# Optimization experiments

Hardware: AMD Instinct MI355X
Metric: run time of the kernel (lower is better)

The kernel has to match this reference:

```python
import jax, jax.numpy as jnp
import numpy as np

EPS = 1e-6
INPUTS = 1836
LABELS = 159
NUM_VALS = 2
HIDDEN = 1024
BATCH = 8192
ITERS = 20          # cfg.inference.iterations
INF_LR = 1.0        # cfg.inference.learning_rate (sqrt decay)
ENT_COEF = 1.0      # cfg.entropy_coef


def setup_inputs() -> dict:
    key = jax.random.key(0)
    ks = jax.random.split(key, 8)
    f32 = jnp.float32
    xs = jax.random.normal(ks[0], (BATCH, INPUTS), f32)
    # feature MLP: 1836 -> 150 -> 150 -> 159 (weights ~ N(0, 2/fan_in), bias 0)
    Wf1 = jax.random.normal(ks[1], (150, INPUTS), f32) * np.sqrt(2.0 / INPUTS).astype(np.float32)
    bf1 = jnp.zeros((150,), f32)
    Wf2 = jax.random.normal(ks[2], (150, 150), f32) * np.sqrt(2.0 / 150).astype(np.float32)
    bf2 = jnp.zeros((150,), f32)
    Wf3 = jax.random.normal(ks[3], (LABELS, 150), f32) * np.sqrt(2.0 / 150).astype(np.float32)
    bf3 = jnp.zeros((LABELS,), f32)
    # global energy net: Linear(159->1024, no bias), Softplus, Linear(1024->1, no bias)
    Wg1 = jax.random.normal(ks[4], (HIDDEN, LABELS), f32) * (1.0 / np.sqrt(LABELS)).astype(np.float32)
    Wg2 = jax.random.normal(ks[5], (1, HIDDEN), f32) * (1.0 / np.sqrt(HIDDEN)).astype(np.float32)
    return dict(xs=xs, Wf1=Wf1, bf1=bf1, Wf2=Wf2, bf2=bf2, Wf3=Wf3, bf3=bf3, Wg1=Wg1, Wg2=Wg2)


def _init_pred(batch_size):
    # _random_probabilities: sorted-uniform stick-breaking, shared across the batch
    x = jax.random.uniform(jax.random.key(1), (LABELS, NUM_VALS + 1), jnp.float32)
    x = x.at[:, 0].set(0.0).at[:, -1].set(1.0)
    x = jnp.sort(x, axis=1)
    p = x[:, 1:] - x[:, :-1]                       # (LABELS, NUM_VALS), rows sum to 1
    return jnp.broadcast_to(p[None], (batch_size, LABELS, NUM_VALS))


def reference(xs, Wf1, bf1, Wf2, bf2, Wf3, bf3, Wg1, Wg2):
    # feature energy network -> potentials (B, LABELS, 2), channel 0 is zero
    h = jax.nn.relu(xs @ Wf1.T + bf1)
    h = jax.nn.relu(h @ Wf2.T + bf2)
    logits = h @ Wf3.T + bf3                        # (B, LABELS)
    potentials = jnp.stack([jnp.zeros_like(logits), logits], axis=-1)  # (B, LABELS, 2)

    def energy_sum(pred):
        # sum over batch of: <pred, potentials> + Wg2 softplus(Wg1 pred[:,:,1]) - c*H-term
        ge = jnp.sum(pred * potentials)
        le = jnp.sum(jax.nn.softplus(pred[:, :, 1] @ Wg1.T) @ Wg2.T)
        ent = jnp.sum(pred * jnp.log(pred + EPS))
        return ge + le - ENT_COEF * ent

    egrad = jax.grad(energy_sum)

    def step(pred, it):
        g = egrad(pred)                             # (B, LABELS, NUM_VALS)
        lr = INF_LR / jnp.sqrt(it.astype(jnp.float32))
        lg = lr * g
        m = jnp.max(lg, axis=-1, keepdims=True)     # stabilized multiplicative update
        p = pred * jnp.exp(lg - m)
        p = p / (jnp.sum(p, axis=-1, keepdims=True) + EPS)
        return p, None

    pred0 = _init_pred(xs.shape[0])
    pred, _ = jax.lax.scan(step, pred0, jnp.arange(1, ITERS))
    return pred
```

## Files before the change

### kernel.cpp

```cpp
#include <hip/hip_runtime.h>
#include <hip/hip_bf16.h>
#include <math.h>

#define EPSF 1e-6f
#define NLBL 159
#define NLP  160
#define HID  1024
#define BATCH 8192
#define MROWS 32
#define PBS  168
#define SBS  1044
#define K1   1836
#define K1P  1856
#define NF   150
#define NFP  160

typedef __attribute__((ext_vector_type(8))) short short8v;
typedef __attribute__((ext_vector_type(4))) float f32x4;

__device__ inline ushort f2bf(float f) {
  __hip_bfloat16 h = __float2bfloat16(f);
  return *reinterpret_cast<ushort*>(&h);
}
__device__ inline float bf2f(ushort u) {
  unsigned v = ((unsigned)u) << 16;
  return __uint_as_float(v);
}
__device__ inline float rcpf(float x) { return __builtin_amdgcn_rcpf(x); }
__device__ inline float sigmoidf(float x) { return rcpf(1.0f + __expf(-x)); }

__device__ inline unsigned rotl32(unsigned x, int d){ return (x<<d)|(x>>(32-d)); }

__device__ inline void threefry2x32(unsigned k0, unsigned k1,
                                    unsigned x0, unsigned x1,
                                    unsigned* o0, unsigned* o1) {
  unsigned ks0=k0, ks1=k1, ks2=k0^k1^0x1BD11BDAu;
  x0 += ks0; x1 += ks1;
#define TF_R(r) { x0 += x1; x1 = rotl32(x1,(r)); x1 ^= x0; }
  TF_R(13) TF_R(15) TF_R(26) TF_R(6)  x0 += ks1; x1 += ks2 + 1u;
  TF_R(17) TF_R(29) TF_R(16) TF_R(24) x0 += ks2; x1 += ks0 + 2u;
  TF_R(13) TF_R(15) TF_R(26) TF_R(6)  x0 += ks0; x1 += ks1 + 3u;
  TF_R(17) TF_R(29) TF_R(16) TF_R(24) x0 += ks1; x1 += ks2 + 4u;
  TF_R(13) TF_R(15) TF_R(26) TF_R(6)  x0 += ks2; x1 += ks0 + 5u;
#undef TF_R
  *o0 = x0; *o1 = x1;
}

template<int RELU>
__global__ __launch_bounds__(256) void gemm_xwt(const float* __restrict__ A,
                                                const float* __restrict__ W,
                                                const float* __restrict__ bias,
                                                float* __restrict__ C,
                                                int M, int N, int K) {
  __shared__ float As[32][68];
  __shared__ float Ws[32][68];
  const int tid = threadIdx.x;
  const int m0 = blockIdx.x * 64;
  const int n0 = blockIdx.y * 64;
  const int tn = tid & 15;
  const int tm = tid >> 4;
  float acc[4][4];
#pragma unroll
  for (int i=0;i<4;++i)
#pragma unroll
    for (int j=0;j<4;++j) acc[i][j]=0.f;

  for (int k0 = 0; k0 < K; k0 += 32) {
    __syncthreads();
#pragma unroll
    for (int s2 = 0; s2 < 8; ++s2) {
      int f = tid + s2*256;
      int kk = f & 31, mm = f >> 5;
      int k = k0 + kk;
      float av = 0.f, wvv = 0.f;
      if (k < K) {
        av = A[(size_t)(m0+mm)*K + k];
        int n = n0 + mm;
        if (n < N) wvv = W[(size_t)n*K + k];
      }
      As[kk][mm] = av;
      Ws[kk][mm] = wvv;
    }
    __syncthreads();
    for (int kk=0; kk<32; ++kk) {
      float4 a4 = *(const float4*)&As[kk][tm*4];
      float4 b4 = *(const float4*)&Ws[kk][tn*4];
      float ai[4] = {a4.x,a4.y,a4.z,a4.w};
      float bj[4] = {b4.x,b4.y,b4.z,b4.w};
#pragma unroll
      for (int i=0;i<4;++i)
#pragma unroll
        for (int j=0;j<4;++j) acc[i][j] = fmaf(ai[i], bj[j], acc[i][j]);
    }
  }
#pragma unroll
  for (int i=0;i<4;++i)
#pragma unroll
    for (int j=0;j<4;++j) {
      int m = m0 + tm*4 + i;
      int n = n0 + tn*4 + j;
      if (n < N) {
        float v = acc[i][j] + bias[n];
        if (RELU) v = fmaxf(v, 0.f);
        C[(size_t)m*N + n] = v;
      }
    }
}

__global__ void prep_weights(const float* __restrict__ Wg1,
                             ushort* __restrict__ Wg1b,
                             ushort* __restrict__ Wg1Tb) {
  int idx = blockIdx.x*256 + threadIdx.x;
  if (idx >= HID*NLP) return;
  int h = idx / NLP, l = idx % NLP;
  float v = (l < NLBL) ? Wg1[h*NLBL + l] : 0.f;
  ushort b = f2bf(v);
  Wg1b[h*NLP + l]  = b;
  Wg1Tb[l*HID + h] = b;
}

__global__ void prep_wf1(const float* __restrict__ Wf1,
                         ushort* __restrict__ Wh, ushort* __restrict__ Wl) {
  int idx = blockIdx.x*256 + threadIdx.x;
  if (idx >= NFP*K1P) return;
  int n = idx / K1P, k = idx % K1P;
  float v = (n < NF && k < K1) ? Wf1[n*K1 + k] : 0.f;
  ushort h = f2bf(v);
  Wh[idx] = h;
  Wl[idx] = f2bf(v - bf2f(h));
}

__global__ __launch_bounds__(256) void gemm1_split(
    const float* __restrict__ xs, const ushort* __restrict__ Wh,
    const ushort* __restrict__ Wl, const float* __restrict__ bias,
    float* __restrict__ h1) {
  __shared__ float Asf[32*36];
  const int tid = threadIdx.x;
  const int wv = tid >> 6, lane = tid & 63;
  const int c = lane & 15, g = lane >> 4;
  const int row0 = blockIdx.x * 32;
  const int ntc = (wv < 2) ? 3 : 2;
  const int ntv[3] = {wv, wv + 4, wv + 8};

  f32x4 acc[3][2];
#pragma unroll
  for (int t = 0; t < 3; ++t)
#pragma unroll
    for (int rt = 0; rt < 2; ++rt) acc[t][rt] = (f32x4){0.f,0.f,0.f,0.f};

  const int srow = tid >> 3;
  const int skof = (tid & 7) * 4;

  for (int ks = 0; ks < K1P/32; ++ks) {
    const int k0 = ks * 32;
    const int ksrc = k0 + skof;
    const float4 av = *(const float4*)&xs[(size_t)(row0 + srow)*K1 + ((ksrc < K1) ? ksrc : 0)];
    __syncthreads();
    *(float4*)&Asf[srow*36 + skof] = av;
    __syncthreads();
    short8v ah[2], al[2];
#pragma unroll
    for (int rt = 0; rt < 2; ++rt) {
      const float* ap = &Asf[(rt*16 + c)*36 + g*8];
      float4 x0 = *(const float4*)ap;
      float4 x1 = *(const float4*)(ap + 4);
      float xv[8] = {x0.x,x0.y,x0.z,x0.w,x1.x,x1.y,x1.z,x1.w};
#pragma unroll
      for (int j = 0; j < 8; ++j) {
        ushort hh = f2bf(xv[j]);
        ah[rt][j] = (short)hh;
        al[rt][j] = (short)f2bf(xv[j] - bf2f(hh));
      }
    }
#pragma unroll
    for (int t = 0; t < 3; ++t) {
      if (t >= ntc) break;
      const int n = ntv[t]*16 + c;
      const size_t wo = (size_t)n*K1P + k0 + g*8;
      short8v wh = *(const short8v*)&Wh[wo];
      short8v wl = *(const short8v*)&Wl[wo];
#pragma unroll
      for (int rt = 0; rt < 2; ++rt) {
        acc[t][rt] = __builtin_amdgcn_mfma_f32_16x16x32_bf16(ah[rt], wh, acc[t][rt], 0, 0, 0);
        acc[t][rt] = __builtin_amdgcn_mfma_f32_16x16x32_bf16(ah[rt], wl, acc[t][rt], 0, 0, 0);
        acc[t][rt] = __builtin_amdgcn_mfma_f32_16x16x32_bf16(al[rt], wh, acc[t][rt], 0, 0, 0);
      }
    }
  }
#pragma unroll
  for (int t = 0; t < 3; ++t) {
    if (t >= ntc) break;
    const int n = ntv[t]*16 + c;
    if (n < NF) {
      const float bv = bias[n];
#pragma unroll
      for (int rt = 0; rt < 2; ++rt)
#pragma unroll
        for (int r = 0; r < 4; ++r) {
          int m = row0 + rt*16 + g*4 + r;
          h1[(size_t)m*NF + n] = fmaxf(acc[t][rt][r] + bv, 0.f);
        }
    }
  }
}

__global__ __launch_bounds__(512, 2) void spen_iter_mfma(
    const float* __restrict__ logits,
    const ushort* __restrict__ Wg1b,
    const ushort* __restrict__ Wg1Tb,
    const float* __restrict__ Wg2,
    float* __restrict__ out) {
  __shared__ ushort p1b[MROWS*PBS];
  __shared__ ushort s_b[MROWS*SBS];
  __shared__ float  u_s[NLBL];

  const int tid  = threadIdx.x;
  const int wv   = tid >> 6;
  const int lane = tid & 63;
  const int col  = lane & 15;
  const int kg   = lane >> 4;
  const int row0 = blockIdx.x * MROWS;

  if (tid < NLBL) {
    unsigned i = 3u*(unsigned)tid + 1u;
    unsigned x0, x1; bool use1;
    if (i < 239u) { x0 = i; x1 = (i == 238u) ? 0u : (239u + i); use1 = false; }
    else          { x0 = i - 239u; x1 = i; use1 = true; }
    unsigned o0, o1;
    threefry2x32(0u, 1u, x0, x1, &o0, &o1);
    unsigned bits = use1 ? o1 : o0;
    u_s[tid] = __uint_as_float((bits >> 9) | 0x3f800000u) - 1.0f;
  }
  __syncthreads();
  for (int idx = tid; idx < MROWS*NLP; idx += 512) {
    int m = idx / NLP, l = idx % NLP;
    float p1 = (l < NLBL) ? (1.0f - u_s[l]) : 0.f;
    p1b[m*PBS + l] = f2bf(p1);
  }

  const bool has2 = (wv < 2);
  const int l0 = wv*16 + col;
  const int l1 = 128 + wv*16 + col;
  const bool v1 = has2 && (l1 < NLBL);

  float q0[8], q1[8];
  {
    float u0v = u_s[l0];
    float qi0 = __logf((1.0f - u0v) * rcpf(u0v));
    float qi1 = 0.f;
    if (v1) { float u1v = u_s[l1]; qi1 = __logf((1.0f - u1v) * rcpf(u1v)); }
#pragma unroll
    for (int i = 0; i < 8; ++i) { q0[i] = qi0; q1[i] = qi1; }
  }

  float wg2own[8];
#pragma unroll
  for (int tt = 0; tt < 8; ++tt) wg2own[tt] = Wg2[(wv*8 + tt)*16 + col];

  float lg0[8], lg1[8];
#pragma unroll
  for (int rh = 0; rh < 2; ++rh)
#pragma unroll
    for (int r = 0; r < 4; ++r) {
      int m = row0 + rh*16 + kg*4 + r;
      lg0[rh*4+r] = logits[(size_t)m*NLBL + l0];
      lg1[rh*4+r] = v1 ? logits[(size_t)m*NLBL + l1] : 0.f;
    }

  const ushort* wbase = Wg1b + ((size_t)(wv*8)*16 + col)*NLP + kg*8;

  for (int it = 1; it <= 19; ++it) {
    const float lr = rsqrtf((float)it);
    __syncthreads();
    short8v afr0[5], afr1[5];
#pragma unroll
    for (int kk = 0; kk < 5; ++kk) {
      afr0[kk] = *(const short8v*)&p1b[col*PBS + kk*32 + kg*8];
      afr1[kk] = *(const short8v*)&p1b[(16 + col)*PBS + kk*32 + kg*8];
    }
    short8v wA[2][5];
#pragma unroll
    for (int kk = 0; kk < 5; ++kk) wA[0][kk] = *(const short8v*)(wbase + kk*32);
#pragma unroll
    for (int tt = 0; tt < 8; ++tt) {
      const int cur = tt & 1;
      if (tt < 7) {
        const ushort* wp = wbase + (size_t)((tt + 1)*16)*NLP;
#pragma unroll
        for (int kk = 0; kk < 5; ++kk) wA[cur^1][kk] = *(const short8v*)(wp + kk*32);
      }
      f32x4 a0 = (f32x4){0.f,0.f,0.f,0.f};
      f32x4 a1 = (f32x4){0.f,0.f,0.f,0.f};
#pragma unroll
      for (int kk = 0; kk < 5; ++kk) {
        a0 = __builtin_amdgcn_mfma_f32_16x16x32_bf16(afr0[kk], wA[cur][kk], a0, 0, 0, 0);
        a1 = __builtin_amdgcn_mfma_f32_16x16x32_bf16(afr1[kk], wA[cur][kk], a1, 0, 0, 0);
      }
      const int h = (wv*8 + tt)*16 + col;
      const float wg2v = wg2own[tt];
#pragma unroll
      for (int r = 0; r < 4; ++r) {
        s_b[(kg*4 + r)*SBS + h]      = f2bf(wg2v * sigmoidf(a0[r]));
        s_b[(16 + kg*4 + r)*SBS + h] = f2bf(wg2v * sigmoidf(a1[r]));
      }
    }
    __syncthreads();
    f32x4 bA0 = (f32x4){0.f,0.f,0.f,0.f};
    f32x4 bA1 = (f32x4){0.f,0.f,0.f,0.f};
    f32x4 bB0 = (f32x4){0.f,0.f,0.f,0.f};
    f32x4 bB1 = (f32x4){0.f,0.f,0.f,0.f};
    const ushort* sp0 = &s_b[col*SBS + kg*8];
    const ushort* sp1 = &s_b[(16 + col)*SBS + kg*8];
    const ushort* wt0 = &Wg1Tb[(size_t)l0*HID + kg*8];
    if (has2) {
      const ushort* wt1 = &Wg1Tb[(size_t)l1*HID + kg*8];
#pragma unroll
      for (int kk = 0; kk < 32; ++kk) {
        short8v w0 = *(const short8v*)(wt0 + kk*32);
        short8v w1 = *(const short8v*)(wt1 + kk*32);
        short8v a0 = *(const short8v*)(sp0 + kk*32);
        short8v a1 = *(const short8v*)(sp1 + kk*32);
        bA0 = __builtin_amdgcn_mfma_f32_16x16x32_bf16(a0, w0, bA0, 0, 0, 0);
        bA1 = __builtin_amdgcn_mfma_f32_16x16x32_bf16(a1, w0, bA1, 0, 0, 0);
        bB0 = __builtin_amdgcn_mfma_f32_16x16x32_bf16(a0, w1, bB0, 0, 0, 0);
        bB1 = __builtin_amdgcn_mfma_f32_16x16x32_bf16(a1, w1, bB1, 0, 0, 0);
      }
    } else {
#pragma unroll
      for (int kk = 0; kk < 32; ++kk) {
        short8v w0 = *(const short8v*)(wt0 + kk*32);
        short8v a0 = *(const short8v*)(sp0 + kk*32);
        short8v a1 = *(const short8v*)(sp1 + kk*32);
        bA0 = __builtin_amdgcn_mfma_f32_16x16x32_bf16(a0, w0, bA0, 0, 0, 0);
        bA1 = __builtin_amdgcn_mfma_f32_16x16x32_bf16(a1, w0, bA1, 0, 0, 0);
      }
    }
#define UPDATE_ONE(QARR, IDX, LGV, BK, LL, MM)                               \
    {                                                                        \
      float q = QARR[IDX];                                                   \
      float p1v = sigmoidf(q);                                               \
      float p0v = 1.0f - p1v;                                                \
      float rp1 = rcpf(p1v + EPSF);                                          \
      float rp0 = rcpf(p0v + EPSF);                                          \
      float dlt = (LGV) + (BK) - __logf((p1v + EPSF)*rp0) - p1v*rp1 + p0v*rp0;\
      q += lr*dlt;                                                           \
      QARR[IDX] = q;                                                         \
      p1b[(MM)*PBS + (LL)] = f2bf(sigmoidf(q));                              \
    }
#pragma unroll
    for (int r = 0; r < 4; ++r) {
      const int m0r = kg*4 + r;
      UPDATE_ONE(q0, r, lg0[r], bA0[r], l0, m0r)
      const int m1r = 16 + kg*4 + r;
      UPDATE_ONE(q0, 4 + r, lg0[4 + r], bA1[r], l0, m1r)
    }
    if (v1) {
#pragma unroll
      for (int r = 0; r < 4; ++r) {
        const int m0r = kg*4 + r;
        UPDATE_ONE(q1, r, lg1[r], bB0[r], l1, m0r)
        const int m1r = 16 + kg*4 + r;
        UPDATE_ONE(q1, 4 + r, lg1[4 + r], bB1[r], l1, m1r)
      }
    }
#undef UPDATE_ONE
  }

#pragma unroll
  for (int rh = 0; rh < 2; ++rh)
#pragma unroll
    for (int r = 0; r < 4; ++r) {
      const int row = row0 + rh*16 + kg*4 + r;
      float p1v = sigmoidf(q0[rh*4 + r]);
      size_t o = ((size_t)row*NLBL + l0)*2;
      out[o]   = 1.0f - p1v;
      out[o+1] = p1v;
      if (v1) {
        float p1w = sigmoidf(q1[rh*4 + r]);
        size_t o2 = ((size_t)row*NLBL + l1)*2;
        out[o2]   = 1.0f - p1w;
        out[o2+1] = p1w;
      }
    }
}

extern "C" void kernel_launch(void* const* d_in, const int* in_sizes, int n_in,
                              void* d_out, int out_size, void* d_ws, size_t ws_size,
                              hipStream_t stream) {
  const float* xs  = (const float*)d_in[0];
  const float* Wf1 = (const float*)d_in[1];
  const float* bf1 = (const float*)d_in[2];
  const float* Wf2 = (const float*)d_in[3];
  const float* bf2 = (const float*)d_in[4];
  const float* Wf3 = (const float*)d_in[5];
  const float* bf3 = (const float*)d_in[6];
  const float* Wg1 = (const float*)d_in[7];
  const float* Wg2 = (const float*)d_in[8];
  float* out = (float*)d_out;

  float* h1     = (float*)d_ws;
  float* h2     = h1 + (size_t)BATCH*NF;
  float* logits = h2 + (size_t)BATCH*NF;
  ushort* Wg1b  = (ushort*)(logits + (size_t)BATCH*NLBL);
  ushort* Wg1Tb = Wg1b + (size_t)HID*NLP;
  ushort* Wf1h  = Wg1Tb + (size_t)NLP*HID;
  ushort* Wf1l  = Wf1h + (size_t)NFP*K1P;

  prep_wf1<<<(NFP*K1P + 255)/256, 256, 0, stream>>>(Wf1, Wf1h, Wf1l);
  prep_weights<<<(HID*NLP + 255)/256, 256, 0, stream>>>(Wg1, Wg1b, Wg1Tb);

  gemm1_split<<<BATCH/32, 256, 0, stream>>>(xs, Wf1h, Wf1l, bf1, h1);
  gemm_xwt<1><<<dim3(BATCH/64, 3), 256, 0, stream>>>(h1, Wf2, bf2, h2, BATCH, NF, NF);
  gemm_xwt<0><<<dim3(BATCH/64, 3), 256, 0, stream>>>(h2, Wf3, bf3, logits, BATCH, NLBL, NF);

  spen_iter_mfma<<<BATCH/MROWS, 512, 0, stream>>>(logits, Wg1b, Wg1Tb, Wg2, out);
}
```

Before: 525.5 us.

## Rebalance hidden-tile split across waves and skew weight-load order per block

Phase A's 64 hidden tiles are now split unevenly between waves. The two waves that also carry a second label tile in phase B get only 2 tiles, and the other six get 10 each. This balances the combined MFMA work per wave. Weight loads in both phases are skewed by block index, so blocks running at the same time read different parts of Wg1 and stagger cache and channel pressure. Phase B now prefetches weights in double-buffered chunks of four, which adds register pressure under the existing launch bounds.

Result: slower. 596.5 us (+13.5%).

```diff
diff --git a/kernel.cpp b/kernel.cpp
--- a/kernel.cpp
+++ b/kernel.cpp
@@ -204,6 +204,103 @@
   }
 }
 
+template<int NPAIR>
+__device__ __forceinline__ void phase_a(
+    const ushort* __restrict__ wbase,
+    const float* __restrict__ Wg2,
+    const short8v afr0[5], const short8v afr1[5],
+    ushort* __restrict__ s_b,
+    int col, int kg, int tstart, int pskew)
+{
+  short8v wb[2][2][5];
+  float   wgp[2][2];
+  {
+    const int pv = pskew;
+    const ushort* b0 = wbase + (size_t)((tstart + pv*2)*16)*NLP;
+#pragma unroll
+    for (int kk = 0; kk < 5; ++kk) {
+      wb[0][0][kk] = *(const short8v*)(b0 + kk*32);
+      wb[0][1][kk] = *(const short8v*)(b0 + (size_t)16*NLP + kk*32);
+    }
+    wgp[0][0] = Wg2[(tstart + pv*2)*16 + col];
+    wgp[0][1] = Wg2[(tstart + pv*2 + 1)*16 + col];
+  }
+#pragma unroll
+  for (int p = 0; p < NPAIR; ++p) {
+    const int cur = p & 1;
+    int pv = p + pskew; if (pv >= NPAIR) pv -= NPAIR;
+    if (p + 1 < NPAIR) {
+      int pn = p + 1 + pskew; if (pn >= NPAIR) pn -= NPAIR;
+      const ushort* b1 = wbase + (size_t)((tstart + pn*2)*16)*NLP;
+#pragma unroll
+      for (int kk = 0; kk < 5; ++kk) {
+        wb[cur^1][0][kk] = *(const short8v*)(b1 + kk*32);
+        wb[cur^1][1][kk] = *(const short8v*)(b1 + (size_t)16*NLP + kk*32);
+      }
+      wgp[cur^1][0] = Wg2[(tstart + pn*2)*16 + col];
+      wgp[cur^1][1] = Wg2[(tstart + pn*2 + 1)*16 + col];
+    }
+#pragma unroll
+    for (int i = 0; i < 2; ++i) {
+      f32x4 a0 = (f32x4){0.f,0.f,0.f,0.f};
+      f32x4 a1 = (f32x4){0.f,0.f,0.f,0.f};
+#pragma unroll
+      for (int kk = 0; kk < 5; ++kk) {
+        a0 = __builtin_amdgcn_mfma_f32_16x16x32_bf16(afr0[kk], wb[cur][i][kk], a0, 0, 0, 0);
+        a1 = __builtin_amdgcn_mfma_f32_16x16x32_bf16(afr1[kk], wb[cur][i][kk], a1, 0, 0, 0);
+      }
+      const int h = (tstart + pv*2 + i)*16 + col;
+      const float g = wgp[cur][i];
+#pragma unroll
+      for (int r = 0; r < 4; ++r) {
+        s_b[(kg*4 + r)*SBS + h]      = f2bf(g * sigmoidf(a0[r]));
+        s_b[(16 + kg*4 + r)*SBS + h] = f2bf(g * sigmoidf(a1[r]));
+      }
+    }
+  }
+}
+
+template<int NLT>
+__device__ __forceinline__ void phase_b(
+    const ushort* __restrict__ wt0, const ushort* __restrict__ wt1,
+    const ushort* __restrict__ sp0, const ushort* __restrict__ sp1,
+    int bskew, f32x4 (&acc)[2][2])
+{
+  short8v wr[2][NLT][4];
+  {
+    const int kc = bskew * 4;
+#pragma unroll
+    for (int j = 0; j < 4; ++j) {
+      wr[0][0][j] = *(const short8v*)(wt0 + (kc + j)*32);
+      if (NLT == 2) wr[0][NLT-1][j] = *(const short8v*)(wt1 + (kc + j)*32);
+    }
+  }
+#pragma unroll
+  for (int kb = 0; kb < 8; ++kb) {
+    const int cur = kb & 1;
+    if (kb + 1 < 8) {
+      const int kn = ((kb + 1 + bskew) & 7) * 4;
+#pragma unroll
+      for (int j = 0; j < 4; ++j) {
+        wr[cur^1][0][j] = *(const short8v*)(wt0 + (kn + j)*32);
+        if (NLT == 2) wr[cur^1][NLT-1][j] = *(const short8v*)(wt1 + (kn + j)*32);
+      }
+    }
+    const int kc = ((kb + bskew) & 7) * 4;
+#pragma unroll
+    for (int j = 0; j < 4; ++j) {
+      short8v a0 = *(const short8v*)(sp0 + (kc + j)*32);
+      short8v a1 = *(const short8v*)(sp1 + (kc + j)*32);
+      acc[0][0] = __builtin_amdgcn_mfma_f32_16x16x32_bf16(a0, wr[cur][0][j], acc[0][0], 0, 0, 0);
+      acc[0][1] = __builtin_amdgcn_mfma_f32_16x16x32_bf16(a1, wr[cur][0][j], acc[0][1], 0, 0, 0);
+      if (NLT == 2) {
+        acc[1][0] = __builtin_amdgcn_mfma_f32_16x16x32_bf16(a0, wr[cur][NLT-1][j], acc[1][0], 0, 0, 0);
+        acc[1][1] = __builtin_amdgcn_mfma_f32_16x16x32_bf16(a1, wr[cur][NLT-1][j], acc[1][1], 0, 0, 0);
+      }
+    }
+  }
+}
+
 __global__ __launch_bounds__(512, 2) void spen_iter_mfma(
     const float* __restrict__ logits,
     const ushort* __restrict__ Wg1b,
@@ -220,6 +317,8 @@
   const int col  = lane & 15;
   const int kg   = lane >> 4;
   const int row0 = blockIdx.x * MROWS;
+  const int pskew5 = (int)((blockIdx.x >> 3) % 5u);
+  const int bskew  = (int)((blockIdx.x >> 3) & 7u);
 
   if (tid < NLBL) {
     unsigned i = 3u*(unsigned)tid + 1u;
@@ -242,6 +341,7 @@
   const int l0 = wv*16 + col;
   const int l1 = 128 + wv*16 + col;
   const bool v1 = has2 && (l1 < NLBL);
+  const int tstart = (wv < 2) ? wv*2 : 4 + (wv - 2)*10;
 
   float q0[8], q1[8];
   {
@@ -253,10 +353,6 @@
     for (int i = 0; i < 8; ++i) { q0[i] = qi0; q1[i] = qi1; }
   }
 
-  float wg2own[8];
-#pragma unroll
-  for (int tt = 0; tt < 8; ++tt) wg2own[tt] = Wg2[(wv*8 + tt)*16 + col];
-
   float lg0[8], lg1[8];
 #pragma unroll
   for (int rh = 0; rh < 2; ++rh)
@@ -267,7 +363,11 @@
       lg1[rh*4+r] = v1 ? logits[(size_t)m*NLBL + l1] : 0.f;
     }
 
-  const ushort* wbase = Wg1b + ((size_t)(wv*8)*16 + col)*NLP + kg*8;
+  const ushort* wbase = Wg1b + (size_t)col*NLP + kg*8;
+  const ushort* sp0 = &s_b[col*SBS + kg*8];
+  const ushort* sp1 = &s_b[(16 + col)*SBS + kg*8];
+  const ushort* wt0 = &Wg1Tb[(size_t)l0*HID + kg*8];
+  const ushort* wt1 = &Wg1Tb[(size_t)l1*HID + kg*8];
 
   for (int it = 1; it <= 19; ++it) {
     const float lr = rsqrtf((float)it);
@@ -278,63 +378,16 @@
       afr0[kk] = *(const short8v*)&p1b[col*PBS + kk*32 + kg*8];
       afr1[kk] = *(const short8v*)&p1b[(16 + col)*PBS + kk*32 + kg*8];
     }
-    short8v wA[2][5];
-#pragma unroll
-    for (int kk = 0; kk < 5; ++kk) wA[0][kk] = *(const short8v*)(wbase + kk*32);
-#pragma unroll
-    for (int tt = 0; tt < 8; ++tt) {
-      const int cur = tt & 1;
-      if (tt < 7) {
-        const ushort* wp = wbase + (size_t)((tt + 1)*16)*NLP;
-#pragma unroll
-        for (int kk = 0; kk < 5; ++kk) wA[cur^1][kk] = *(const short8v*)(wp + kk*32);
-      }
-      f32x4 a0 = (f32x4){0.f,0.f,0.f,0.f};
-      f32x4 a1 = (f32x4){0.f,0.f,0.f,0.f};
-#pragma unroll
-      for (int kk = 0; kk < 5; ++kk) {
-        a0 = __builtin_amdgcn_mfma_f32_16x16x32_bf16(afr0[kk], wA[cur][kk], a0, 0, 0, 0);
-        a1 = __builtin_amdgcn_mfma_f32_16x16x32_bf16(afr1[kk], wA[cur][kk], a1, 0, 0, 0);
-      }
-      const int h = (wv*8 + tt)*16 + col;
-      const float wg2v = wg2own[tt];
-#pragma unroll
-      for (int r = 0; r < 4; ++r) {
-        s_b[(kg*4 + r)*SBS + h]      = f2bf(wg2v * sigmoidf(a0[r]));
-        s_b[(16 + kg*4 + r)*SBS + h] = f2bf(wg2v * sigmoidf(a1[r]));
-      }
-    }
-    __syncthreads();
-    f32x4 bA0 = (f32x4){0.f,0.f,0.f,0.f};
-    f32x4 bA1 = (f32x4){0.f,0.f,0.f,0.f};
-    f32x4 bB0 = (f32x4){0.f,0.f,0.f,0.f};
-    f32x4 bB1 = (f32x4){0.f,0.f,0.f,0.f};
-    const ushort* sp0 = &s_b[col*SBS + kg*8];
-    const ushort* sp1 = &s_b[(16 + col)*SBS + kg*8];
-    const ushort* wt0 = &Wg1Tb[(size_t)l0*HID + kg*8];
-    if (has2) {
-      const ushort* wt1 = &Wg1Tb[(size_t)l1*HID + kg*8];
-#pragma unroll
-      for (int kk = 0; kk < 32; ++kk) {
-        short8v w0 = *(const short8v*)(wt0 + kk*32);
-        short8v w1 = *(const short8v*)(wt1 + kk*32);
-        short8v a0 = *(const short8v*)(sp0 + kk*32);
-        short8v a1 = *(const short8v*)(sp1 + kk*32);
-        bA0 = __builtin_amdgcn_mfma_f32_16x16x32_bf16(a0, w0, bA0, 0, 0, 0);
-        bA1 = __builtin_amdgcn_mfma_f32_16x16x32_bf16(a1, w0, bA1, 0, 0, 0);
-        bB0 = __builtin_amdgcn_mfma_f32_16x16x32_bf16(a0, w1, bB0, 0, 0, 0);
-        bB1 = __builtin_amdgcn_mfma_f32_16x16x32_bf16(a1, w1, bB1, 0, 0, 0);
-      }
-    } else {
-#pragma unroll
-      for (int kk = 0; kk < 32; ++kk) {
-        short8v w0 = *(const short8v*)(wt0 + kk*32);
-        short8v a0 = *(const short8v*)(sp0 + kk*32);
-        short8v a1 = *(const short8v*)(sp1 + kk*32);
-        bA0 = __builtin_amdgcn_mfma_f32_16x16x32_bf16(a0, w0, bA0, 0, 0, 0);
-        bA1 = __builtin_amdgcn_mfma_f32_16x16x32_bf16(a1, w0, bA1, 0, 0, 0);
-      }
-    }
+    if (wv < 2) phase_a<1>(wbase, Wg2, afr0, afr1, s_b, col, kg, tstart, 0);
+    else        phase_a<5>(wbase, Wg2, afr0, afr1, s_b, col, kg, tstart, pskew5);
+    __syncthreads();
+    f32x4 acc2[2][2];
+    acc2[0][0] = (f32x4){0.f,0.f,0.f,0.f};
+    acc2[0][1] = (f32x4){0.f,0.f,0.f,0.f};
+    acc2[1][0] = (f32x4){0.f,0.f,0.f,0.f};
+    acc2[1][1] = (f32x4){0.f,0.f,0.f,0.f};
+    if (has2) phase_b<2>(wt0, wt1, sp0, sp1, bskew, acc2);
+    else      phase_b<1>(wt0, wt0, sp0, sp1, bskew, acc2);
 #define UPDATE_ONE(QARR, IDX, LGV, BK, LL, MM)                               \
     {                                                                        \
       float q = QARR[IDX];                                                   \
@@ -350,17 +403,17 @@
 #pragma unroll
     for (int r = 0; r < 4; ++r) {
       const int m0r = kg*4 + r;
-      UPDATE_ONE(q0, r, lg0[r], bA0[r], l0, m0r)
+      UPDATE_ONE(q0, r, lg0[r], acc2[0][0][r], l0, m0r)
       const int m1r = 16 + kg*4 + r;
-      UPDATE_ONE(q0, 4 + r, lg0[4 + r], bA1[r], l0, m1r)
+      UPDATE_ONE(q0, 4 + r, lg0[4 + r], acc2[0][1][r], l0, m1r)
     }
     if (v1) {
 #pragma unroll
       for (int r = 0; r < 4; ++r) {
         const int m0r = kg*4 + r;
-        UPDATE_ONE(q1, r, lg1[r], bB0[r], l1, m0r)
+        UPDATE_ONE(q1, r, lg1[r], acc2[1][0][r], l1, m0r)
         const int m1r = 16 + kg*4 + r;
-        UPDATE_ONE(q1, 4 + r, lg1[4 + r], bB1[r], l1, m1r)
+        UPDATE_ONE(q1, 4 + r, lg1[4 + r], acc2[1][1][r], l1, m1r)
       }
     }
 #undef UPDATE_ONE
```

## Rotate weight-tile order per block and double-buffer transposed weight loads

Applied to the files above, without the earlier changes.

Each group of blocks starts its sweep over Wg1 tiles and Wg1T K-chunks at a different rotated offset, so concurrent blocks do not all hit the same global weight addresses at once. The second GEMM's weight loads move from a fully unrolled loop to an explicit double-buffered prefetch of 4-chunk groups. Launch bounds drop from 2 to 1 block per SM, giving the compiler more registers at the cost of occupancy. Rotation indices add modulo address arithmetic, and the extra buffered registers may push register pressure up.

Measured after the change: 783.6 us. +49.1%, slower.

```diff
diff --git a/kernel.cpp b/kernel.cpp
--- a/kernel.cpp
+++ b/kernel.cpp
@@ -204,7 +204,7 @@
   }
 }
 
-__global__ __launch_bounds__(512, 2) void spen_iter_mfma(
+__global__ __launch_bounds__(512, 1) void spen_iter_mfma(
     const float* __restrict__ logits,
     const ushort* __restrict__ Wg1b,
     const ushort* __restrict__ Wg1Tb,
@@ -220,6 +220,9 @@
   const int col  = lane & 15;
   const int kg   = lane >> 4;
   const int row0 = blockIdx.x * MROWS;
+  const unsigned ublk = blockIdx.x >> 3;
+  const int rT = (int)(ublk & 7u);
+  const int rB = (int)((ublk * 5u) & 7u);
 
   if (tid < NLBL) {
     unsigned i = 3u*(unsigned)tid + 1u;
@@ -255,7 +258,10 @@
 
   float wg2own[8];
 #pragma unroll
-  for (int tt = 0; tt < 8; ++tt) wg2own[tt] = Wg2[(wv*8 + tt)*16 + col];
+  for (int j = 0; j < 8; ++j) {
+    int tj = (j + rT) & 7;
+    wg2own[j] = Wg2[(wv*8 + tj)*16 + col];
+  }
 
   float lg0[8], lg1[8];
 #pragma unroll
@@ -267,7 +273,11 @@
       lg1[rh*4+r] = v1 ? logits[(size_t)m*NLBL + l1] : 0.f;
     }
 
-  const ushort* wbase = Wg1b + ((size_t)(wv*8)*16 + col)*NLP + kg*8;
+  const ushort* wvbase = Wg1b + ((size_t)(wv*128) + col)*NLP + kg*8;
+  const ushort* sp0 = &s_b[col*SBS + kg*8];
+  const ushort* sp1 = &s_b[(16 + col)*SBS + kg*8];
+  const ushort* wt0 = &Wg1Tb[(size_t)l0*HID + kg*8];
+  const ushort* wt1 = &Wg1Tb[(size_t)l1*HID + kg*8];
 
   for (int it = 1; it <= 19; ++it) {
     const float lr = rsqrtf((float)it);
@@ -279,15 +289,19 @@
       afr1[kk] = *(const short8v*)&p1b[(16 + col)*PBS + kk*32 + kg*8];
     }
     short8v wA[2][5];
-#pragma unroll
-    for (int kk = 0; kk < 5; ++kk) wA[0][kk] = *(const short8v*)(wbase + kk*32);
-#pragma unroll
-    for (int tt = 0; tt < 8; ++tt) {
-      const int cur = tt & 1;
-      if (tt < 7) {
-        const ushort* wp = wbase + (size_t)((tt + 1)*16)*NLP;
-#pragma unroll
-        for (int kk = 0; kk < 5; ++kk) wA[cur^1][kk] = *(const short8v*)(wp + kk*32);
+    {
+      const ushort* p = wvbase + (size_t)rT*16*NLP;
+#pragma unroll
+      for (int kk = 0; kk < 5; ++kk) wA[0][kk] = *(const short8v*)(p + kk*32);
+    }
+#pragma unroll
+    for (int j = 0; j < 8; ++j) {
+      const int cur = j & 1;
+      if (j < 7) {
+        const int tn = (j + 1 + rT) & 7;
+        const ushort* p = wvbase + (size_t)tn*16*NLP;
+#pragma unroll
+        for (int kk = 0; kk < 5; ++kk) wA[cur^1][kk] = *(const short8v*)(p + kk*32);
       }
       f32x4 a0 = (f32x4){0.f,0.f,0.f,0.f};
       f32x4 a1 = (f32x4){0.f,0.f,0.f,0.f};
@@ -296,12 +310,13 @@
         a0 = __builtin_amdgcn_mfma_f32_16x16x32_bf16(afr0[kk], wA[cur][kk], a0, 0, 0, 0);
         a1 = __builtin_amdgcn_mfma_f32_16x16x32_bf16(afr1[kk], wA[cur][kk], a1, 0, 0, 0);
       }
-      const int h = (wv*8 + tt)*16 + col;
-      const float wg2v = wg2own[tt];
+      const int tj = (j + rT) & 7;
+      const int h = (wv*8 + tj)*16 + col;
+      const float g = wg2own[j];
 #pragma unroll
       for (int r = 0; r < 4; ++r) {
-        s_b[(kg*4 + r)*SBS + h]      = f2bf(wg2v * sigmoidf(a0[r]));
-        s_b[(16 + kg*4 + r)*SBS + h] = f2bf(wg2v * sigmoidf(a1[r]));
+        s_b[(kg*4 + r)*SBS + h]      = f2bf(g * sigmoidf(a0[r]));
+        s_b[(16 + kg*4 + r)*SBS + h] = f2bf(g * sigmoidf(a1[r]));
       }
     }
     __syncthreads();
@@ -309,30 +324,65 @@
     f32x4 bA1 = (f32x4){0.f,0.f,0.f,0.f};
     f32x4 bB0 = (f32x4){0.f,0.f,0.f,0.f};
     f32x4 bB1 = (f32x4){0.f,0.f,0.f,0.f};
-    const ushort* sp0 = &s_b[col*SBS + kg*8];
-    const ushort* sp1 = &s_b[(16 + col)*SBS + kg*8];
-    const ushort* wt0 = &Wg1Tb[(size_t)l0*HID + kg*8];
     if (has2) {
-      const ushort* wt1 = &Wg1Tb[(size_t)l1*HID + kg*8];
-#pragma unroll
-      for (int kk = 0; kk < 32; ++kk) {
-        short8v w0 = *(const short8v*)(wt0 + kk*32);
-        short8v w1 = *(const short8v*)(wt1 + kk*32);
-        short8v a0 = *(const short8v*)(sp0 + kk*32);
-        short8v a1 = *(const short8v*)(sp1 + kk*32);
-        bA0 = __builtin_amdgcn_mfma_f32_16x16x32_bf16(a0, w0, bA0, 0, 0, 0);
-        bA1 = __builtin_amdgcn_mfma_f32_16x16x32_bf16(a1, w0, bA1, 0, 0, 0);
-        bB0 = __builtin_amdgcn_mfma_f32_16x16x32_bf16(a0, w1, bB0, 0, 0, 0);
-        bB1 = __builtin_amdgcn_mfma_f32_16x16x32_bf16(a1, w1, bB1, 0, 0, 0);
+      short8v wr[2][2][4];
+      {
+        const int ab = rB;
+#pragma unroll
+        for (int j = 0; j < 4; ++j) {
+          wr[0][0][j] = *(const short8v*)(wt0 + (ab*4 + j)*32);
+          wr[0][1][j] = *(const short8v*)(wt1 + (ab*4 + j)*32);
+        }
+      }
+#pragma unroll
+      for (int b = 0; b < 8; ++b) {
+        const int cur = b & 1;
+        if (b < 7) {
+          const int an = (b + 1 + rB) & 7;
+#pragma unroll
+          for (int j = 0; j < 4; ++j) {
+            wr[cur^1][0][j] = *(const short8v*)(wt0 + (an*4 + j)*32);
+            wr[cur^1][1][j] = *(const short8v*)(wt1 + (an*4 + j)*32);
+          }
+        }
+        const int ab = (b + rB) & 7;
+#pragma unroll
+        for (int j = 0; j < 4; ++j) {
+          const int kk = ab*4 + j;
+          short8v a0 = *(const short8v*)(sp0 + kk*32);
+          short8v a1 = *(const short8v*)(sp1 + kk*32);
+          bA0 = __builtin_amdgcn_mfma_f32_16x16x32_bf16(a0, wr[cur][0][j], bA0, 0, 0, 0);
+          bA1 = __builtin_amdgcn_mfma_f32_16x16x32_bf16(a1, wr[cur][0][j], bA1, 0, 0, 0);
+          bB0 = __builtin_amdgcn_mfma_f32_16x16x32_bf16(a0, wr[cur][1][j], bB0, 0, 0, 0);
+          bB1 = __builtin_amdgcn_mfma_f32_16x16x32_bf16(a1, wr[cur][1][j], bB1, 0, 0, 0);
+        }
       }
     } else {
-#pragma unroll
-      for (int kk = 0; kk < 32; ++kk) {
-        short8v w0 = *(const short8v*)(wt0 + kk*32);
-        short8v a0 = *(const short8v*)(sp0 + kk*32);
-        short8v a1 = *(const short8v*)(sp1 + kk*32);
-        bA0 = __builtin_amdgcn_mfma_f32_16x16x32_bf16(a0, w0, bA0, 0, 0, 0);
-        bA1 = __builtin_amdgcn_mfma_f32_16x16x32_bf16(a1, w0, bA1, 0, 0, 0);
+      short8v wr[2][4];
+      {
+        const int ab = rB;
+#pragma unroll
+        for (int j = 0; j < 4; ++j)
+          wr[0][j] = *(const short8v*)(wt0 + (ab*4 + j)*32);
+      }
+#pragma unroll
+      for (int b = 0; b < 8; ++b) {
+        const int cur = b & 1;
+        if (b < 7) {
+          const int an = (b + 1 + rB) & 7;
+#pragma unroll
+          for (int j = 0; j < 4; ++j)
+            wr[cur^1][j] = *(const short8v*)(wt0 + (an*4 + j)*32);
+        }
+        const int ab = (b + rB) & 7;
+#pragma unroll
+        for (int j = 0; j < 4; ++j) {
+          const int kk = ab*4 + j;
+          short8v a0 = *(const short8v*)(sp0 + kk*32);
+          short8v a1 = *(const short8v*)(sp1 + kk*32);
+          bA0 = __builtin_amdgcn_mfma_f32_16x16x32_bf16(a0, wr[cur][j], bA0, 0, 0, 0);
+          bA1 = __builtin_amdgcn_mfma_f32_16x16x32_bf16(a1, wr[cur][j], bA1, 0, 0, 0);
+        }
       }
     }
 #define UPDATE_ONE(QARR, IDX, LGV, BK, LL, MM)                               \
```

## Use 16 waves per block with load-balanced split of hidden and label work

Applied to the files above, without the earlier changes.

The iteration kernel moves from 8 to 16 waves per block. Ten waves each own one 16-label tile for phase B and the update, and they take a smaller share of phase A hidden tiles (2 each, versus 7 or 8 for the other waves) to even out the load. Phase B now double-buffers the Wg1T weight fragments in registers, and the first batch is issued before the barrier so its load latency overlaps the wait. Each wave gets fewer VGPRs under launch bounds of 1024 threads, so register pressure and spills are a risk. LDS use per block stays near 74KB, which limits occupancy to about two blocks per CU.

New measurement: 866.6 us. +64.9%, slower.

```diff
diff --git a/kernel.cpp b/kernel.cpp
--- a/kernel.cpp
+++ b/kernel.cpp
@@ -204,7 +204,46 @@
   }
 }
 
-__global__ __launch_bounds__(512, 2) void spen_iter_mfma(
+template<int NT>
+__device__ __forceinline__ void phase_a16(
+    const ushort* __restrict__ wbase0,
+    const float* __restrict__ Wg2,
+    const short8v afr0[5], const short8v afr1[5],
+    ushort* __restrict__ s_b,
+    int col, int kg, int tstart)
+{
+  short8v wA[2][5];
+#pragma unroll
+  for (int kk = 0; kk < 5; ++kk) wA[0][kk] = *(const short8v*)(wbase0 + kk*32);
+  float g = Wg2[tstart*16 + col];
+#pragma unroll
+  for (int j = 0; j < NT; ++j) {
+    const int cur = j & 1;
+    float gn = g;
+    if (j < NT - 1) {
+      const ushort* p = wbase0 + (size_t)((j + 1)*16)*NLP;
+#pragma unroll
+      for (int kk = 0; kk < 5; ++kk) wA[cur^1][kk] = *(const short8v*)(p + kk*32);
+      gn = Wg2[(tstart + j + 1)*16 + col];
+    }
+    f32x4 a0 = (f32x4){0.f,0.f,0.f,0.f};
+    f32x4 a1 = (f32x4){0.f,0.f,0.f,0.f};
+#pragma unroll
+    for (int kk = 0; kk < 5; ++kk) {
+      a0 = __builtin_amdgcn_mfma_f32_16x16x32_bf16(afr0[kk], wA[cur][kk], a0, 0, 0, 0);
+      a1 = __builtin_amdgcn_mfma_f32_16x16x32_bf16(afr1[kk], wA[cur][kk], a1, 0, 0, 0);
+    }
+    const int h = (tstart + j)*16 + col;
+#pragma unroll
+    for (int r = 0; r < 4; ++r) {
+      s_b[(kg*4 + r)*SBS + h]      = f2bf(g * sigmoidf(a0[r]));
+      s_b[(16 + kg*4 + r)*SBS + h] = f2bf(g * sigmoidf(a1[r]));
+    }
+    g = gn;
+  }
+}
+
+__global__ __launch_bounds__(1024, 4) void spen_iter_mfma(
     const float* __restrict__ logits,
     const ushort* __restrict__ Wg1b,
     const ushort* __restrict__ Wg1Tb,
@@ -232,42 +271,38 @@
     u_s[tid] = __uint_as_float((bits >> 9) | 0x3f800000u) - 1.0f;
   }
   __syncthreads();
-  for (int idx = tid; idx < MROWS*NLP; idx += 512) {
+  for (int idx = tid; idx < MROWS*NLP; idx += 1024) {
     int m = idx / NLP, l = idx % NLP;
     float p1 = (l < NLBL) ? (1.0f - u_s[l]) : 0.f;
     p1b[m*PBS + l] = f2bf(p1);
   }
 
-  const bool has2 = (wv < 2);
+  const bool owner = (wv < 10);
   const int l0 = wv*16 + col;
-  const int l1 = 128 + wv*16 + col;
-  const bool v1 = has2 && (l1 < NLBL);
-
-  float q0[8], q1[8];
+  const bool vcell = owner && (l0 < NLBL);
+  const int tstart = (wv < 10) ? 2*wv : ((wv < 14) ? 20 + 7*(wv - 10) : 48 + 8*(wv - 14));
+
+  float q0[8];
   {
-    float u0v = u_s[l0];
-    float qi0 = __logf((1.0f - u0v) * rcpf(u0v));
-    float qi1 = 0.f;
-    if (v1) { float u1v = u_s[l1]; qi1 = __logf((1.0f - u1v) * rcpf(u1v)); }
-#pragma unroll
-    for (int i = 0; i < 8; ++i) { q0[i] = qi0; q1[i] = qi1; }
-  }
-
-  float wg2own[8];
-#pragma unroll
-  for (int tt = 0; tt < 8; ++tt) wg2own[tt] = Wg2[(wv*8 + tt)*16 + col];
-
-  float lg0[8], lg1[8];
+    float qi = 0.f;
+    if (vcell) { float uv = u_s[l0]; qi = __logf((1.0f - uv) * rcpf(uv)); }
+#pragma unroll
+    for (int i = 0; i < 8; ++i) q0[i] = qi;
+  }
+
+  float lg0[8];
 #pragma unroll
   for (int rh = 0; rh < 2; ++rh)
 #pragma unroll
     for (int r = 0; r < 4; ++r) {
       int m = row0 + rh*16 + kg*4 + r;
-      lg0[rh*4+r] = logits[(size_t)m*NLBL + l0];
-      lg1[rh*4+r] = v1 ? logits[(size_t)m*NLBL + l1] : 0.f;
-    }
-
-  const ushort* wbase = Wg1b + ((size_t)(wv*8)*16 + col)*NLP + kg*8;
+      lg0[rh*4 + r] = vcell ? logits[(size_t)m*NLBL + l0] : 0.f;
+    }
+
+  const ushort* wbaseA = Wg1b + ((size_t)(tstart*16) + col)*NLP + kg*8;
+  const ushort* sp0 = &s_b[col*SBS + kg*8];
+  const ushort* sp1 = &s_b[(16 + col)*SBS + kg*8];
+  const ushort* wt0 = &Wg1Tb[(size_t)l0*HID + kg*8];
 
   for (int it = 1; it <= 19; ++it) {
     const float lr = rsqrtf((float)it);
@@ -278,110 +313,68 @@
       afr0[kk] = *(const short8v*)&p1b[col*PBS + kk*32 + kg*8];
       afr1[kk] = *(const short8v*)&p1b[(16 + col)*PBS + kk*32 + kg*8];
     }
-    short8v wA[2][5];
-#pragma unroll
-    for (int kk = 0; kk < 5; ++kk) wA[0][kk] = *(const short8v*)(wbase + kk*32);
-#pragma unroll
-    for (int tt = 0; tt < 8; ++tt) {
-      const int cur = tt & 1;
-      if (tt < 7) {
-        const ushort* wp = wbase + (size_t)((tt + 1)*16)*NLP;
-#pragma unroll
-        for (int kk = 0; kk < 5; ++kk) wA[cur^1][kk] = *(const short8v*)(wp + kk*32);
-      }
-      f32x4 a0 = (f32x4){0.f,0.f,0.f,0.f};
-      f32x4 a1 = (f32x4){0.f,0.f,0.f,0.f};
-#pragma unroll
-      for (int kk = 0; kk < 5; ++kk) {
-        a0 = __builtin_amdgcn_mfma_f32_16x16x32_bf16(afr0[kk], wA[cur][kk], a0, 0, 0, 0);
-        a1 = __builtin_amdgcn_mfma_f32_16x16x32_bf16(afr1[kk], wA[cur][kk], a1, 0, 0, 0);
-      }
-      const int h = (wv*8 + tt)*16 + col;
-      const float wg2v = wg2own[tt];
+    if (wv < 10)      phase_a16<2>(wbaseA, Wg2, afr0, afr1, s_b, col, kg, tstart);
+    else if (wv < 14) phase_a16<7>(wbaseA, Wg2, afr0, afr1, s_b, col, kg, tstart);
+    else              phase_a16<8>(wbaseA, Wg2, afr0, afr1, s_b, col, kg, tstart);
+    short8v wr[2][8];
+    if (owner) {
+#pragma unroll
+      for (int j = 0; j < 8; ++j) wr[0][j] = *(const short8v*)(wt0 + j*32);
+    }
+    __syncthreads();
+    f32x4 b0 = (f32x4){0.f,0.f,0.f,0.f};
+    f32x4 b1 = (f32x4){0.f,0.f,0.f,0.f};
+    if (owner) {
+#pragma unroll
+      for (int b = 0; b < 4; ++b) {
+        const int cur = b & 1;
+        if (b < 3) {
+#pragma unroll
+          for (int j = 0; j < 8; ++j)
+            wr[cur^1][j] = *(const short8v*)(wt0 + ((b + 1)*8 + j)*32);
+        }
+#pragma unroll
+        for (int j = 0; j < 8; ++j) {
+          const int kk = b*8 + j;
+          short8v a0 = *(const short8v*)(sp0 + kk*32);
+          short8v a1 = *(const short8v*)(sp1 + kk*32);
+          b0 = __builtin_amdgcn_mfma_f32_16x16x32_bf16(a0, wr[cur][j], b0, 0, 0, 0);
+          b1 = __builtin_amdgcn_mfma_f32_16x16x32_bf16(a1, wr[cur][j], b1, 0, 0, 0);
+        }
+      }
+#define UPDATE_ONE(IDX, LGV, BK, MM)                                         \
+      {                                                                      \
+        float q = q0[IDX];                                                   \
+        float p1v = sigmoidf(q);                                             \
+        float p0v = 1.0f - p1v;                                              \
+        float rp1 = rcpf(p1v + EPSF);                                        \
+        float rp0 = rcpf(p0v + EPSF);                                        \
+        float dlt = (LGV) + (BK) - __logf((p1v + EPSF)*rp0) - p1v*rp1 + p0v*rp0;\
+        q += lr*dlt;                                                         \
+        q0[IDX] = q;                                                         \
+        if (vcell) p1b[(MM)*PBS + l0] = f2bf(sigmoidf(q));                   \
+      }
 #pragma unroll
       for (int r = 0; r < 4; ++r) {
-        s_b[(kg*4 + r)*SBS + h]      = f2bf(wg2v * sigmoidf(a0[r]));
-        s_b[(16 + kg*4 + r)*SBS + h] = f2bf(wg2v * sigmoidf(a1[r]));
-      }
-    }
-    __syncthreads();
-    f32x4 bA0 = (f32x4){0.f,0.f,0.f,0.f};
-    f32x4 bA1 = (f32x4){0.f,0.f,0.f,0.f};
-    f32x4 bB0 = (f32x4){0.f,0.f,0.f,0.f};
-    f32x4 bB1 = (f32x4){0.f,0.f,0.f,0.f};
-    const ushort* sp0 = &s_b[col*SBS + kg*8];
-    const ushort* sp1 = &s_b[(16 + col)*SBS + kg*8];
-    const ushort* wt0 = &Wg1Tb[(size_t)l0*HID + kg*8];
-    if (has2) {
-      const ushort* wt1 = &Wg1Tb[(size_t)l1*HID + kg*8];
-#pragma unroll
-      for (int kk = 0; kk < 32; ++kk) {
-        short8v w0 = *(const short8v*)(wt0 + kk*32);
-        short8v w1 = *(const short8v*)(wt1 + kk*32);
-        short8v a0 = *(const short8v*)(sp0 + kk*32);
-        short8v a1 = *(const short8v*)(sp1 + kk*32);
-        bA0 = __builtin_amdgcn_mfma_f32_16x16x32_bf16(a0, w0, bA0, 0, 0, 0);
-        bA1 = __builtin_amdgcn_mfma_f32_16x16x32_bf16(a1, w0, bA1, 0, 0, 0);
-        bB0 = __builtin_amdgcn_mfma_f32_16x16x32_bf16(a0, w1, bB0, 0, 0, 0);
-        bB1 = __builtin_amdgcn_mfma_f32_16x16x32_bf16(a1, w1, bB1, 0, 0, 0);
-      }
-    } else {
-#pragma unroll
-      for (int kk = 0; kk < 32; ++kk) {
-        short8v w0 = *(const short8v*)(wt0 + kk*32);
-        short8v a0 = *(const short8v*)(sp0 + kk*32);
-        short8v a1 = *(const short8v*)(sp1 + kk*32);
-        bA0 = __builtin_amdgcn_mfma_f32_16x16x32_bf16(a0, w0, bA0, 0, 0, 0);
-        bA1 = __builtin_amdgcn_mfma_f32_16x16x32_bf16(a1, w0, bA1, 0, 0, 0);
-      }
-    }
-#define UPDATE_ONE(QARR, IDX, LGV, BK, LL, MM)                               \
-    {                                                                        \
-      float q = QARR[IDX];                                                   \
-      float p1v = sigmoidf(q);                                               \
-      float p0v = 1.0f - p1v;                                                \
-      float rp1 = rcpf(p1v + EPSF);                                          \
-      float rp0 = rcpf(p0v + EPSF);                                          \
-      float dlt = (LGV) + (BK) - __logf((p1v + EPSF)*rp0) - p1v*rp1 + p0v*rp0;\
-      q += lr*dlt;                                                           \
-      QARR[IDX] = q;                                                         \
-      p1b[(MM)*PBS + (LL)] = f2bf(sigmoidf(q));                              \
-    }
-#pragma unroll
-    for (int r = 0; r < 4; ++r) {
-      const int m0r = kg*4 + r;
-      UPDATE_ONE(q0, r, lg0[r], bA0[r], l0, m0r)
-      const int m1r = 16 + kg*4 + r;
-      UPDATE_ONE(q0, 4 + r, lg0[4 + r], bA1[r], l0, m1r)
-    }
-    if (v1) {
+        UPDATE_ONE(r,     lg0[r],     b0[r], kg*4 + r)
+        UPDATE_ONE(4 + r, lg0[4 + r], b1[r], 16 + kg*4 + r)
+      }
+#undef UPDATE_ONE
+    }
+  }
+
+  if (vcell) {
+#pragma unroll
+    for (int rh = 0; rh < 2; ++rh)
 #pragma unroll
       for (int r = 0; r < 4; ++r) {
-        const int m0r = kg*4 + r;
-        UPDATE_ONE(q1, r, lg1[r], bB0[r], l1, m0r)
-        const int m1r = 16 + kg*4 + r;
-        UPDATE_ONE(q1, 4 + r, lg1[4 + r], bB1[r], l1, m1r)
-      }
-    }
-#undef UPDATE_ONE
-  }
-
-#pragma unroll
-  for (int rh = 0; rh < 2; ++rh)
-#pragma unroll
-    for (int r = 0; r < 4; ++r) {
-      const int row = row0 + rh*16 + kg*4 + r;
-      float p1v = sigmoidf(q0[rh*4 + r]);
-      size_t o = ((size_t)row*NLBL + l0)*2;
-      out[o]   = 1.0f - p1v;
-      out[o+1] = p1v;
-      if (v1) {
-        float p1w = sigmoidf(q1[rh*4 + r]);
-        size_t o2 = ((size_t)row*NLBL + l1)*2;
-        out[o2]   = 1.0f - p1w;
-        out[o2+1] = p1w;
-      }
-    }
+        const int row = row0 + rh*16 + kg*4 + r;
+        float p1v = sigmoidf(q0[rh*4 + r]);
+        size_t o = ((size_t)row*NLBL + l0)*2;
+        out[o]   = 1.0f - p1v;
+        out[o+1] = p1v;
+      }
+  }
 }
 
 extern "C" void kernel_launch(void* const* d_in, const int* in_sizes, int n_in,
@@ -413,5 +406,5 @@
   gemm_xwt<1><<<dim3(BATCH/64, 3), 256, 0, stream>>>(h1, Wf2, bf2, h2, BATCH, NF, NF);
   gemm_xwt<0><<<dim3(BATCH/64, 3), 256, 0, stream>>>(h2, Wf3, bf3, logits, BATCH, NLBL, NF);
 
-  spen_iter_mfma<<<BATCH/MROWS, 512, 0, stream>>>(logits, Wg1b, Wg1Tb, Wg2, out);
-}
+  spen_iter_mfma<<<BATCH/MROWS, 1024, 0, stream>>>(logits, Wg1b, Wg1Tb, Wg2, out);
+}
```
